# Kernel tuning notes

Measured on AMD Instinct MI355X. Metric: run time of the kernel, lower is better.

Reference implementation:

```python
import jax, jax.numpy as jnp
import numpy as np

B, S, DM, H, D = 2, 1024, 1024, 16, 64  # batch, seq, d_model, heads, head_dim


def setup_inputs() -> dict:
    key = jax.random.key(0)
    ks = jax.random.split(key, 16)
    sc = 1.0 / np.sqrt(DM)
    scd = 1.0 / np.sqrt(D)
    return {
        "hidden_states": jax.random.normal(ks[0], (B, S, DM), dtype=jnp.float32),
        # frozen base_attn projections
        "Wq": jax.random.normal(ks[1], (DM, DM), dtype=jnp.float32) * sc,
        "bq": jnp.zeros((DM,), dtype=jnp.float32),
        "Wk": jax.random.normal(ks[2], (DM, DM), dtype=jnp.float32) * sc,
        "bk": jnp.zeros((DM,), dtype=jnp.float32),
        "Wv": jax.random.normal(ks[3], (DM, DM), dtype=jnp.float32) * sc,
        "bv": jnp.zeros((DM,), dtype=jnp.float32),
        "Wo": jax.random.normal(ks[4], (DM, DM), dtype=jnp.float32) * sc,
        "bo": jnp.zeros((DM,), dtype=jnp.float32),
        # trainable hedgehog feature maps (per-head Linear(head_dim, head_dim))
        "Wfq": jax.random.normal(ks[5], (D, D), dtype=jnp.float32) * scd,
        "bfq": jnp.zeros((D,), dtype=jnp.float32),
        "Wfk": jax.random.normal(ks[6], (D, D), dtype=jnp.float32) * scd,
        "bfk": jnp.zeros((D,), dtype=jnp.float32),
    }


def _heads(x):
    # (B, S, DM) -> (B, H, S, D)
    return x.reshape(B, S, H, D).transpose(0, 2, 1, 3)


def _feature_map(x, W, b):
    # HedgehogFeatureMap: Linear then concat(exp(x), exp(-x)) along last dim
    y = jnp.einsum('bhsd,ed->bhse', x, W) + b
    return jnp.concatenate([jnp.exp(y), jnp.exp(-y)], axis=-1)  # (B,H,S,2D)


def reference(hidden_states, Wq, bq, Wk, bk, Wv, bv, Wo, bo, Wfq, bfq, Wfk, bfk):
    # base_attn: standard multi-head softmax attention with output_attentions=True
    q = _heads(hidden_states @ Wq.T + bq)
    k = _heads(hidden_states @ Wk.T + bk)
    v = _heads(hidden_states @ Wv.T + bv)
    scores = jnp.einsum('bhmd,bhnd->bhmn', q, k) / jnp.sqrt(jnp.float32(D))
    true_attns = jax.nn.softmax(scores, axis=-1)  # (B,H,S,S)
    ctx = jnp.einsum('bhmn,bhnd->bhmd', true_attns, v)
    outputs = ctx.transpose(0, 2, 1, 3).reshape(B, S, DM) @ Wo.T + bo

    # hedgehog path: feature maps on q/k then sum-normalized quadratic attention
    fq = _feature_map(q, Wfq, bfq)
    fk = _feature_map(k, Wfk, bfk)
    qk = jnp.einsum('bhmd,bhnd->bhmn', fq, fk)
    pred_attns = qk / jnp.sum(qk, axis=-1, keepdims=True)
    return (outputs, pred_attns, true_attns)
```

## Files before the change

kernel.cpp:

```cpp
#include <hip/hip_runtime.h>
#include <math.h>

constexpr int B_ = 2, S_ = 1024, DM_ = 1024, NH_ = 16, HD_ = 64;
constexpr long SD = (long)S_ * DM_;
constexpr long SS = (long)S_ * S_;

typedef _Float16 half8 __attribute__((ext_vector_type(8)));
typedef _Float16 half4 __attribute__((ext_vector_type(4)));
typedef float floatx4 __attribute__((ext_vector_type(4)));

__device__ __forceinline__ void gl_lds16(const void* g, void* l) {
    __builtin_amdgcn_global_load_lds(
        (const __attribute__((address_space(1))) void*)g,
        (__attribute__((address_space(3))) void*)l, 16, 0, 0);
}

__global__ __launch_bounds__(256) void cvt_all(
    const float* __restrict__ hs,  const float* __restrict__ Wq,
    const float* __restrict__ Wk,  const float* __restrict__ Wv,
    const float* __restrict__ Wo,  const float* __restrict__ Wfq,
    const float* __restrict__ Wfk,
    _Float16* __restrict__ hsH, _Float16* __restrict__ WqH,
    _Float16* __restrict__ WkH, _Float16* __restrict__ WvH,
    _Float16* __restrict__ WoH, _Float16* __restrict__ WfqH,
    _Float16* __restrict__ WfkH)
{
    long i = (long)blockIdx.x * 256 + threadIdx.x;
    const float* src; _Float16* dst; long off;
    if (i < 524288)       { src = hs;  dst = hsH;  off = i; }
    else if (i < 786432)  { src = Wq;  dst = WqH;  off = i - 524288; }
    else if (i < 1048576) { src = Wk;  dst = WkH;  off = i - 786432; }
    else if (i < 1310720) { src = Wv;  dst = WvH;  off = i - 1048576; }
    else if (i < 1572864) { src = Wo;  dst = WoH;  off = i - 1310720; }
    else if (i < 1573888) { src = Wfq; dst = WfqH; off = i - 1572864; }
    else                  { src = Wfk; dst = WfkH; off = i - 1573888; }
    float4 v = ((const float4*)src)[off];
    half4 h = { (_Float16)v.x, (_Float16)v.y, (_Float16)v.z, (_Float16)v.w };
    ((half4*)dst)[off] = h;
}

template <int BM, int BN, int WM, int WN>
__global__ __launch_bounds__(256) void mm_nt(
    const _Float16* __restrict__ Ap, const _Float16* __restrict__ Wp,
    const float* __restrict__ bias, const float* __restrict__ skp,
    float* __restrict__ Cf,
    _Float16* __restrict__ Ch, int K, int lda, int ldw, int ldc,
    long sAb, long sAh, long sWb, long sWh, long sCb, long sCh,
    float scale, int mode)
{
    constexpr int MI = WM / 16, NI = WN / 16;
    const int z = blockIdx.z, b = z / NH_, h = z % NH_;
    const int wave = threadIdx.x >> 6, lane = threadIdx.x & 63;
    const int m0 = blockIdx.y * BM, n0 = blockIdx.x * BN;
    const int wm = (wave >> 1) * WM, wn = (wave & 1) * WN;
    const int r16 = lane & 15, quad = lane >> 4;

    const _Float16* Az = Ap + (long)b * sAb + (long)h * sAh;
    const _Float16* Wz = Wp + (long)b * sWb + (long)h * sWh;

    __shared__ __align__(16) _Float16 As[2 * BM * 32];
    __shared__ __align__(16) _Float16 Bs[2 * BN * 32];
    __shared__ float skz[128];
    __shared__ float rsinvs[BM];

    if (skp) {
        if (threadIdx.x < 128) {
            float s = 0.f;
#pragma unroll
            for (int m = 0; m < 16; ++m)
                s += skp[((long)z * 16 + m) * 128 + threadIdx.x];
            skz[threadIdx.x] = s;
        }
        __syncthreads();
        if (threadIdx.x < BM) {
            const _Float16* p = Az + (long)(m0 + threadIdx.x) * lda;
            float acc = 0.f;
#pragma unroll
            for (int d0 = 0; d0 < 128; d0 += 8) {
                half8 v = *(const half8*)(p + d0);
#pragma unroll
                for (int j = 0; j < 8; ++j)
                    acc = fmaf((float)v[j], skz[d0 + j], acc);
            }
            rsinvs[threadIdx.x] = 1.f / acc;
        }
    }

    floatx4 acc[MI][NI];
#pragma unroll
    for (int i = 0; i < MI; ++i)
#pragma unroll
        for (int j = 0; j < NI; ++j)
#pragma unroll
            for (int r = 0; r < 4; ++r) acc[i][j][r] = 0.f;

    for (int k0 = 0; k0 < K; k0 += 64) {
#pragma unroll
        for (int hf = 0; hf < 2; ++hf) {
#pragma unroll
            for (int c = wave * (BM / 64); c < (wave + 1) * (BM / 64); ++c) {
                const _Float16* g = Az + (long)(m0 + c * 16 + (lane >> 2)) * lda
                                    + k0 + hf * 32 + (lane & 3) * 8;
                gl_lds16(g, &As[hf * BM * 32 + c * 512]);
            }
#pragma unroll
            for (int c = wave * (BN / 64); c < (wave + 1) * (BN / 64); ++c) {
                const _Float16* g = Wz + (long)(n0 + c * 16 + (lane >> 2)) * ldw
                                    + k0 + hf * 32 + (lane & 3) * 8;
                gl_lds16(g, &Bs[hf * BN * 32 + c * 512]);
            }
        }
        __syncthreads();

#pragma unroll
        for (int hf = 0; hf < 2; ++hf) {
            half8 af[MI], bf8[NI];
#pragma unroll
            for (int i = 0; i < MI; ++i)
                af[i] = *(const half8*)&As[hf * BM * 32
                                           + (wm + i * 16 + r16) * 32 + quad * 8];
#pragma unroll
            for (int j = 0; j < NI; ++j)
                bf8[j] = *(const half8*)&Bs[hf * BN * 32
                                            + (wn + j * 16 + r16) * 32 + quad * 8];
#pragma unroll
            for (int i = 0; i < MI; ++i)
#pragma unroll
                for (int j = 0; j < NI; ++j)
                    acc[i][j] = __builtin_amdgcn_mfma_f32_16x16x32_f16(
                        af[i], bf8[j], acc[i][j], 0, 0, 0);
        }
        __syncthreads();
    }

    const long cb = (long)b * sCb + (long)h * sCh;
#pragma unroll
    for (int i = 0; i < MI; ++i) {
#pragma unroll
        for (int j = 0; j < NI; ++j) {
#pragma unroll
            for (int r = 0; r < 4; ++r) {
                int row = m0 + wm + i * 16 + quad * 4 + r;
                int col = n0 + wn + j * 16 + r16;
                float v = acc[i][j][r] * scale;
                if (bias) v += bias[col];
                if (skp) v *= rsinvs[row - m0];
                if (mode == 0)
                    __builtin_nontemporal_store(v, &Cf[cb + (long)row * ldc + col]);
                else
                    Ch[cb + (long)row * ldc + col] = (_Float16)v;
            }
        }
    }
}

__global__ __launch_bounds__(256) void qkv_proj(
    const _Float16* __restrict__ hsH,
    const _Float16* __restrict__ W0, const _Float16* __restrict__ W1,
    const _Float16* __restrict__ W2,
    const float* __restrict__ b0, const float* __restrict__ b1,
    const float* __restrict__ b2,
    _Float16* __restrict__ QH, _Float16* __restrict__ KH,
    _Float16* __restrict__ VtH)
{
    const int z = blockIdx.z;
    const _Float16* W = (z == 0) ? W0 : (z == 1) ? W1 : W2;
    const float* bias = (z == 0) ? b0 : (z == 1) ? b1 : b2;

    const int wave = threadIdx.x >> 6, lane = threadIdx.x & 63;
    const int m0 = blockIdx.y * 64, n0 = blockIdx.x * 128;
    const int wm = (wave >> 1) * 32, wn = (wave & 1) * 64;
    const int r16 = lane & 15, quad = lane >> 4;

    __shared__ __align__(16) _Float16 As[2 * 64 * 32];
    __shared__ __align__(16) _Float16 Bs[2 * 128 * 32];

    floatx4 acc[2][4];
#pragma unroll
    for (int i = 0; i < 2; ++i)
#pragma unroll
        for (int j = 0; j < 4; ++j)
#pragma unroll
            for (int r = 0; r < 4; ++r) acc[i][j][r] = 0.f;

    for (int k0 = 0; k0 < 1024; k0 += 64) {
#pragma unroll
        for (int hf = 0; hf < 2; ++hf) {
            const _Float16* ga = hsH + (long)(m0 + wave * 16 + (lane >> 2)) * 1024
                                 + k0 + hf * 32 + (lane & 3) * 8;
            gl_lds16(ga, &As[hf * 2048 + wave * 512]);
#pragma unroll
            for (int c = wave * 2; c < wave * 2 + 2; ++c) {
                const _Float16* gb = W + (long)(n0 + c * 16 + (lane >> 2)) * 1024
                                     + k0 + hf * 32 + (lane & 3) * 8;
                gl_lds16(gb, &Bs[hf * 4096 + c * 512]);
            }
        }
        __syncthreads();

#pragma unroll
        for (int hf = 0; hf < 2; ++hf) {
            half8 af[2], bf8[4];
#pragma unroll
            for (int i = 0; i < 2; ++i)
                af[i] = *(const half8*)&As[hf * 2048
                                           + (wm + i * 16 + r16) * 32 + quad * 8];
#pragma unroll
            for (int j = 0; j < 4; ++j)
                bf8[j] = *(const half8*)&Bs[hf * 4096
                                            + (wn + j * 16 + r16) * 32 + quad * 8];
#pragma unroll
            for (int i = 0; i < 2; ++i)
#pragma unroll
                for (int j = 0; j < 4; ++j)
                    acc[i][j] = __builtin_amdgcn_mfma_f32_16x16x32_f16(
                        af[i], bf8[j], acc[i][j], 0, 0, 0);
        }
        __syncthreads();
    }

    _Float16* dst = (z == 0) ? QH : KH;
#pragma unroll
    for (int i = 0; i < 2; ++i) {
#pragma unroll
        for (int j = 0; j < 4; ++j) {
#pragma unroll
            for (int r = 0; r < 4; ++r) {
                int row = m0 + wm + i * 16 + quad * 4 + r;
                int col = n0 + wn + j * 16 + r16;
                float v = acc[i][j][r] + bias[col];
                if (z < 2) {
                    dst[(long)row * 1024 + col] = (_Float16)v;
                } else {
                    int bb = row >> 10, s = row & 1023;
                    int hh = col >> 6, d = col & 63;
                    VtH[((((long)bb * 16 + hh) * 64 + d) << 10) | s] = (_Float16)v;
                }
            }
        }
    }
}

__global__ __launch_bounds__(512) void attn_fused(
    const _Float16* __restrict__ Q, const _Float16* __restrict__ K,
    const _Float16* __restrict__ Vt, float* __restrict__ trueA,
    _Float16* __restrict__ ctx)
{
    const int z = blockIdx.y, b = z >> 4, h = z & 15;
    const int m0 = blockIdx.x * 32;
    const int wave = threadIdx.x >> 6, lane = threadIdx.x & 63;
    const int r16 = lane & 15, quad = lane >> 4;
    const int c0 = wave * 128;

    __shared__ __align__(16) _Float16 Ps[32 * 1024];
    float* redmx = (float*)Ps;
    float* redsm = (float*)Ps + 256;

    const _Float16* Qb = Q + (long)b * SD + h * 64;
    const _Float16* Kb = K + (long)b * SD + h * 64;

    half8 af[2][2];
#pragma unroll
    for (int mi = 0; mi < 2; ++mi)
#pragma unroll
        for (int ks = 0; ks < 2; ++ks)
            af[mi][ks] = *(const half8*)&Qb[(long)(m0 + mi * 16 + r16) * DM_
                                            + ks * 32 + quad * 8];

    floatx4 acc[2][8];
#pragma unroll
    for (int mi = 0; mi < 2; ++mi)
#pragma unroll
        for (int nj = 0; nj < 8; ++nj)
#pragma unroll
            for (int r = 0; r < 4; ++r) acc[mi][nj][r] = 0.f;

#pragma unroll
    for (int ks = 0; ks < 2; ++ks) {
#pragma unroll
        for (int nj = 0; nj < 8; ++nj) {
            half8 bf = *(const half8*)&Kb[(long)(c0 + nj * 16 + r16) * DM_
                                          + ks * 32 + quad * 8];
            acc[0][nj] = __builtin_amdgcn_mfma_f32_16x16x32_f16(
                af[0][ks], bf, acc[0][nj], 0, 0, 0);
            acc[1][nj] = __builtin_amdgcn_mfma_f32_16x16x32_f16(
                af[1][ks], bf, acc[1][nj], 0, 0, 0);
        }
    }

    float rmx[2][4];
#pragma unroll
    for (int mi = 0; mi < 2; ++mi)
#pragma unroll
        for (int r = 0; r < 4; ++r) {
            float m = acc[mi][0][r];
#pragma unroll
            for (int nj = 1; nj < 8; ++nj) m = fmaxf(m, acc[mi][nj][r]);
#pragma unroll
            for (int o = 1; o <= 8; o <<= 1) m = fmaxf(m, __shfl_xor(m, o, 64));
            rmx[mi][r] = m;
        }
    if (r16 == 0) {
#pragma unroll
        for (int mi = 0; mi < 2; ++mi)
#pragma unroll
            for (int r = 0; r < 4; ++r)
                redmx[wave * 32 + mi * 16 + quad * 4 + r] = rmx[mi][r];
    }
    __syncthreads();
    float mx[2][4];
#pragma unroll
    for (int mi = 0; mi < 2; ++mi)
#pragma unroll
        for (int r = 0; r < 4; ++r) {
            float m = redmx[mi * 16 + quad * 4 + r];
#pragma unroll
            for (int w = 1; w < 8; ++w)
                m = fmaxf(m, redmx[w * 32 + mi * 16 + quad * 4 + r]);
            mx[mi][r] = m;
        }

    float rsm[2][4];
#pragma unroll
    for (int mi = 0; mi < 2; ++mi)
#pragma unroll
        for (int r = 0; r < 4; ++r) {
            float s = 0.f;
#pragma unroll
            for (int nj = 0; nj < 8; ++nj) {
                float p = __expf((acc[mi][nj][r] - mx[mi][r]) * 0.125f);
                acc[mi][nj][r] = p;
                s += p;
            }
#pragma unroll
            for (int o = 1; o <= 8; o <<= 1) s += __shfl_xor(s, o, 64);
            rsm[mi][r] = s;
        }
    if (r16 == 0) {
#pragma unroll
        for (int mi = 0; mi < 2; ++mi)
#pragma unroll
            for (int r = 0; r < 4; ++r)
                redsm[wave * 32 + mi * 16 + quad * 4 + r] = rsm[mi][r];
    }
    __syncthreads();
    float inv[2][4];
#pragma unroll
    for (int mi = 0; mi < 2; ++mi)
#pragma unroll
        for (int r = 0; r < 4; ++r) {
            float s = 0.f;
#pragma unroll
            for (int w = 0; w < 8; ++w)
                s += redsm[w * 32 + mi * 16 + quad * 4 + r];
            inv[mi][r] = 1.f / s;
        }
    __syncthreads();

    float* Ta = trueA + (long)z * SS + (long)m0 * S_;
#pragma unroll
    for (int mi = 0; mi < 2; ++mi) {
#pragma unroll
        for (int r = 0; r < 4; ++r) {
            const int row = mi * 16 + quad * 4 + r;
            const int sw = (row & 7) << 3;
            const float iv = inv[mi][r];
#pragma unroll
            for (int nj = 0; nj < 8; ++nj) {
                const int col = c0 + nj * 16 + r16;
                const float v = acc[mi][nj][r] * iv;
                __builtin_nontemporal_store(v, &Ta[(long)row * S_ + col]);
                Ps[row * 1024 + (col ^ sw)] = (_Float16)v;
            }
        }
    }
    __syncthreads();

    const int mi = wave >> 2, d0 = (wave & 3) * 16;
    const _Float16* Vb = Vt + ((long)z * 64 + d0 + r16) * (long)S_;
    floatx4 c2;
#pragma unroll
    for (int r = 0; r < 4; ++r) c2[r] = 0.f;

    const int swz = (r16 & 7) << 3;
#pragma unroll 8
    for (int k0 = 0; k0 < 1024; k0 += 32) {
        half8 pa = *(const half8*)&Ps[(mi * 16 + r16) * 1024
                                      + ((k0 + quad * 8) ^ swz)];
        half8 vf = *(const half8*)&Vb[k0 + quad * 8];
        c2 = __builtin_amdgcn_mfma_f32_16x16x32_f16(pa, vf, c2, 0, 0, 0);
    }

    _Float16* Cb = ctx + (long)b * SD + h * 64;
#pragma unroll
    for (int r = 0; r < 4; ++r) {
        const int srow = m0 + mi * 16 + quad * 4 + r;
        Cb[(long)srow * DM_ + d0 + r16] = (_Float16)c2[r];
    }
}

__global__ __launch_bounds__(256) void feat_map2(
    const _Float16* __restrict__ QH, const _Float16* __restrict__ KH,
    const _Float16* __restrict__ Wfq, const _Float16* __restrict__ Wfk,
    const float* __restrict__ bfq, const float* __restrict__ bfk,
    _Float16* __restrict__ fqH, _Float16* __restrict__ fkH,
    float* __restrict__ skp)
{
    const int which = blockIdx.z;
    const _Float16* Xh = which ? KH : QH;
    const _Float16* Wf = which ? Wfk : Wfq;
    const float* bf    = which ? bfk : bfq;
    _Float16* outH     = which ? fkH : fqH;

    const int z = blockIdx.y, b = z >> 4, h = z & 15;
    const int mb = blockIdx.x, m0 = mb * 64;
    __shared__ float Xs[64][65];
    __shared__ float Ws[64][65];
    __shared__ float red[16][128];
    const _Float16* Xb = Xh + (long)b * SD + h * 64;
    for (int i = threadIdx.x; i < 4096; i += 256) {
        int r = i >> 6, c = i & 63;
        Xs[r][c] = (float)Xb[(long)(m0 + r) * 1024 + c];
        Ws[r][c] = (float)Wf[i];
    }
    __syncthreads();
    const int tmg = threadIdx.x >> 4;
    const int tm = tmg * 4, tn = (threadIdx.x & 15) * 4;
    float acc[4][4] = {{0.f}};
    for (int k = 0; k < 64; ++k) {
        float xv[4], wv[4];
#pragma unroll
        for (int i = 0; i < 4; ++i) xv[i] = Xs[tm + i][k];
#pragma unroll
        for (int j = 0; j < 4; ++j) wv[j] = Ws[tn + j][k];
#pragma unroll
        for (int i = 0; i < 4; ++i)
#pragma unroll
            for (int j = 0; j < 4; ++j) acc[i][j] = fmaf(xv[i], wv[j], acc[i][j]);
    }
    float sp[4] = {0.f, 0.f, 0.f, 0.f}, sn[4] = {0.f, 0.f, 0.f, 0.f};
#pragma unroll
    for (int i = 0; i < 4; ++i) {
        long base = ((long)z * S_ + m0 + tm + i) * 128;
#pragma unroll
        for (int j = 0; j < 4; ++j) {
            float y = acc[i][j] + bf[tn + j];
            float ep = expf(y), en = expf(-y);
            outH[base + tn + j]      = (_Float16)ep;
            outH[base + 64 + tn + j] = (_Float16)en;
            sp[j] += ep; sn[j] += en;
        }
    }
    if (which) {
#pragma unroll
        for (int j = 0; j < 4; ++j) {
            red[tmg][tn + j]      = sp[j];
            red[tmg][64 + tn + j] = sn[j];
        }
        __syncthreads();
        if (threadIdx.x < 128) {
            float s = 0.f;
#pragma unroll
            for (int g = 0; g < 16; ++g) s += red[g][threadIdx.x];
            skp[((long)z * 16 + mb) * 128 + threadIdx.x] = s;
        }
    }
}

extern "C" void kernel_launch(void* const* d_in, const int* in_sizes, int n_in,
                              void* d_out, int out_size, void* d_ws, size_t ws_size,
                              hipStream_t stream)
{
    (void)in_sizes; (void)n_in; (void)out_size; (void)ws_size;

    const float* hs  = (const float*)d_in[0];
    const float* Wq  = (const float*)d_in[1];
    const float* bq  = (const float*)d_in[2];
    const float* Wk  = (const float*)d_in[3];
    const float* bk  = (const float*)d_in[4];
    const float* Wv  = (const float*)d_in[5];
    const float* bv  = (const float*)d_in[6];
    const float* Wo  = (const float*)d_in[7];
    const float* bo  = (const float*)d_in[8];
    const float* Wfq = (const float*)d_in[9];
    const float* bfq = (const float*)d_in[10];
    const float* Wfk = (const float*)d_in[11];
    const float* bfk = (const float*)d_in[12];

    float* out0  = (float*)d_out;
    float* pred  = out0 + (long)B_ * S_ * DM_;
    float* trueA = pred + (long)B_ * NH_ * S_ * S_;

    _Float16* hsH  = (_Float16*)d_ws;
    _Float16* WqH  = hsH + 2 * 1024 * 1024;
    _Float16* WkH  = WqH + 1024 * 1024;
    _Float16* WvH  = WkH + 1024 * 1024;
    _Float16* WoH  = WvH + 1024 * 1024;
    _Float16* WfqH = WoH + 1024 * 1024;
    _Float16* WfkH = WfqH + 4096;
    _Float16* QH   = WfkH + 4096;
    _Float16* KH   = QH + 2 * 1024 * 1024;
    _Float16* VtH  = KH + 2 * 1024 * 1024;
    _Float16* ctxH = VtH + 2 * 1024 * 1024;
    _Float16* fqH  = ctxH + 2 * 1024 * 1024;
    _Float16* fkH  = fqH + (long)B_ * NH_ * S_ * 128;

    float* skp = (float*)WqH;

    const dim3 blk(256);

    cvt_all<<<6152, blk, 0, stream>>>(
        hs, Wq, Wk, Wv, Wo, Wfq, Wfk,
        hsH, WqH, WkH, WvH, WoH, WfqH, WfkH);

    qkv_proj<<<dim3(8, 32, 3), blk, 0, stream>>>(
        hsH, WqH, WkH, WvH, bq, bk, bv, QH, KH, VtH);

    attn_fused<<<dim3(32, 32), dim3(512), 0, stream>>>(
        QH, KH, VtH, trueA, ctxH);

    mm_nt<64, 64, 32, 32><<<dim3(16, 32, 1), blk, 0, stream>>>(
        ctxH, WoH, bo, nullptr, out0, nullptr, 1024, 1024, 1024, 1024,
        0, 0, 0, 0, 0, 0, 1.f, 0);

    feat_map2<<<dim3(16, 32, 2), blk, 0, stream>>>(
        QH, KH, WfqH, WfkH, bfq, bfk, fqH, fkH, skp);

    mm_nt<128, 128, 64, 64><<<dim3(8, 8, 32), blk, 0, stream>>>(
        fqH, fkH, nullptr, skp, pred, nullptr, 128, 128, 128, 1024,
        (long)16 * S_ * 128, (long)S_ * 128,
        (long)16 * S_ * 128, (long)S_ * 128,
        16 * SS, SS, 1.f, 0);
}
```

Baseline: 457.3 us.

## Swap MFMA operand order to get row-contiguous outputs and vectorized stores

Swaps the A/B operands of the MFMA calls in the GEMM, QKV projection and attention kernels, so each lane holds four consecutive columns of one row instead of four rows of one column. The epilogues become 16-byte float4 nontemporal stores and 8-byte half4 stores in place of scalar stores, and the softmax row reductions are reorganized to match (per-lane reduction plus two cross-quad shuffles instead of four shuffles per row). This targets store-bandwidth and instruction overhead, which matter most for the large fp32 attention-probability outputs. The transposed V store in the QKV kernel stays scalar.

Measured after the change: 448.8 us. Within noise of the previous version (-1.8%).

```diff
diff --git a/kernel.cpp b/kernel.cpp
--- a/kernel.cpp
+++ b/kernel.cpp
@@ -13,6 +13,10 @@
     __builtin_amdgcn_global_load_lds(
         (const __attribute__((address_space(1))) void*)g,
         (__attribute__((address_space(3))) void*)l, 16, 0, 0);
+}
+
+__device__ __forceinline__ void nt_store4(const floatx4& v, float* p) {
+    __builtin_nontemporal_store(v, (floatx4*)p);
 }
 
 __global__ __launch_bounds__(256) void cvt_all(
@@ -128,7 +132,7 @@
 #pragma unroll
                 for (int j = 0; j < NI; ++j)
                     acc[i][j] = __builtin_amdgcn_mfma_f32_16x16x32_f16(
-                        af[i], bf8[j], acc[i][j], 0, 0, 0);
+                        bf8[j], af[i], acc[i][j], 0, 0, 0);
         }
         __syncthreads();
     }
@@ -136,19 +140,28 @@
     const long cb = (long)b * sCb + (long)h * sCh;
 #pragma unroll
     for (int i = 0; i < MI; ++i) {
+        const int row = m0 + wm + i * 16 + r16;
+        const float rs = skp ? rsinvs[row - m0] : 1.f;
 #pragma unroll
         for (int j = 0; j < NI; ++j) {
-#pragma unroll
-            for (int r = 0; r < 4; ++r) {
-                int row = m0 + wm + i * 16 + quad * 4 + r;
-                int col = n0 + wn + j * 16 + r16;
-                float v = acc[i][j][r] * scale;
-                if (bias) v += bias[col];
-                if (skp) v *= rsinvs[row - m0];
-                if (mode == 0)
-                    __builtin_nontemporal_store(v, &Cf[cb + (long)row * ldc + col]);
-                else
-                    Ch[cb + (long)row * ldc + col] = (_Float16)v;
+            const int col = n0 + wn + j * 16 + quad * 4;
+            floatx4 v;
+#pragma unroll
+            for (int r = 0; r < 4; ++r) v[r] = acc[i][j][r] * scale;
+            if (bias) {
+                float4 bv = *(const float4*)&bias[col];
+                v[0] += bv.x; v[1] += bv.y; v[2] += bv.z; v[3] += bv.w;
+            }
+            if (skp) {
+#pragma unroll
+                for (int r = 0; r < 4; ++r) v[r] *= rs;
+            }
+            if (mode == 0) {
+                nt_store4(v, &Cf[cb + (long)row * ldc + col]);
+            } else {
+                half4 hv = { (_Float16)v[0], (_Float16)v[1],
+                             (_Float16)v[2], (_Float16)v[3] };
+                *(half4*)&Ch[cb + (long)row * ldc + col] = hv;
             }
         }
     }
@@ -214,7 +227,7 @@
 #pragma unroll
                 for (int j = 0; j < 4; ++j)
                     acc[i][j] = __builtin_amdgcn_mfma_f32_16x16x32_f16(
-                        af[i], bf8[j], acc[i][j], 0, 0, 0);
+                        bf8[j], af[i], acc[i][j], 0, 0, 0);
         }
         __syncthreads();
     }
@@ -222,20 +235,25 @@
     _Float16* dst = (z == 0) ? QH : KH;
 #pragma unroll
     for (int i = 0; i < 2; ++i) {
+        const int row = m0 + wm + i * 16 + r16;
 #pragma unroll
         for (int j = 0; j < 4; ++j) {
-#pragma unroll
-            for (int r = 0; r < 4; ++r) {
-                int row = m0 + wm + i * 16 + quad * 4 + r;
-                int col = n0 + wn + j * 16 + r16;
-                float v = acc[i][j][r] + bias[col];
-                if (z < 2) {
-                    dst[(long)row * 1024 + col] = (_Float16)v;
-                } else {
-                    int bb = row >> 10, s = row & 1023;
-                    int hh = col >> 6, d = col & 63;
-                    VtH[((((long)bb * 16 + hh) * 64 + d) << 10) | s] = (_Float16)v;
-                }
+            const int col = n0 + wn + j * 16 + quad * 4;
+            float4 bv = *(const float4*)&bias[col];
+            float v0 = acc[i][j][0] + bv.x, v1 = acc[i][j][1] + bv.y;
+            float v2 = acc[i][j][2] + bv.z, v3 = acc[i][j][3] + bv.w;
+            if (z < 2) {
+                half4 hv = { (_Float16)v0, (_Float16)v1,
+                             (_Float16)v2, (_Float16)v3 };
+                *(half4*)&dst[(long)row * 1024 + col] = hv;
+            } else {
+                const int bb = row >> 10, s = row & 1023;
+                const int hh = col >> 6, d0 = col & 63;
+                float vv[4] = { v0, v1, v2, v3 };
+#pragma unroll
+                for (int r = 0; r < 4; ++r)
+                    VtH[((((long)bb * 16 + hh) * 64 + d0 + r) << 10) | s] =
+                        (_Float16)vv[r];
             }
         }
     }
@@ -259,12 +277,12 @@
     const _Float16* Qb = Q + (long)b * SD + h * 64;
     const _Float16* Kb = K + (long)b * SD + h * 64;
 
-    half8 af[2][2];
+    half8 qf[2][2];
 #pragma unroll
     for (int mi = 0; mi < 2; ++mi)
 #pragma unroll
         for (int ks = 0; ks < 2; ++ks)
-            af[mi][ks] = *(const half8*)&Qb[(long)(m0 + mi * 16 + r16) * DM_
+            qf[mi][ks] = *(const half8*)&Qb[(long)(m0 + mi * 16 + r16) * DM_
                                             + ks * 32 + quad * 8];
 
     floatx4 acc[2][8];
@@ -279,99 +297,91 @@
     for (int ks = 0; ks < 2; ++ks) {
 #pragma unroll
         for (int nj = 0; nj < 8; ++nj) {
-            half8 bf = *(const half8*)&Kb[(long)(c0 + nj * 16 + r16) * DM_
+            half8 kf = *(const half8*)&Kb[(long)(c0 + nj * 16 + r16) * DM_
                                           + ks * 32 + quad * 8];
             acc[0][nj] = __builtin_amdgcn_mfma_f32_16x16x32_f16(
-                af[0][ks], bf, acc[0][nj], 0, 0, 0);
+                kf, qf[0][ks], acc[0][nj], 0, 0, 0);
             acc[1][nj] = __builtin_amdgcn_mfma_f32_16x16x32_f16(
-                af[1][ks], bf, acc[1][nj], 0, 0, 0);
-        }
-    }
-
-    float rmx[2][4];
-#pragma unroll
-    for (int mi = 0; mi < 2; ++mi)
-#pragma unroll
-        for (int r = 0; r < 4; ++r) {
-            float m = acc[mi][0][r];
-#pragma unroll
-            for (int nj = 1; nj < 8; ++nj) m = fmaxf(m, acc[mi][nj][r]);
-#pragma unroll
-            for (int o = 1; o <= 8; o <<= 1) m = fmaxf(m, __shfl_xor(m, o, 64));
-            rmx[mi][r] = m;
-        }
-    if (r16 == 0) {
-#pragma unroll
-        for (int mi = 0; mi < 2; ++mi)
-#pragma unroll
-            for (int r = 0; r < 4; ++r)
-                redmx[wave * 32 + mi * 16 + quad * 4 + r] = rmx[mi][r];
+                kf, qf[1][ks], acc[1][nj], 0, 0, 0);
+        }
+    }
+
+    float mxl[2];
+#pragma unroll
+    for (int mi = 0; mi < 2; ++mi) {
+        float m = acc[mi][0][0];
+#pragma unroll
+        for (int nj = 0; nj < 8; ++nj)
+#pragma unroll
+            for (int r = 0; r < 4; ++r) m = fmaxf(m, acc[mi][nj][r]);
+        m = fmaxf(m, __shfl_xor(m, 16, 64));
+        m = fmaxf(m, __shfl_xor(m, 32, 64));
+        mxl[mi] = m;
+    }
+    if (quad == 0) {
+        redmx[wave * 32 + r16]      = mxl[0];
+        redmx[wave * 32 + 16 + r16] = mxl[1];
     }
     __syncthreads();
-    float mx[2][4];
-#pragma unroll
-    for (int mi = 0; mi < 2; ++mi)
-#pragma unroll
-        for (int r = 0; r < 4; ++r) {
-            float m = redmx[mi * 16 + quad * 4 + r];
-#pragma unroll
-            for (int w = 1; w < 8; ++w)
-                m = fmaxf(m, redmx[w * 32 + mi * 16 + quad * 4 + r]);
-            mx[mi][r] = m;
-        }
-
-    float rsm[2][4];
-#pragma unroll
-    for (int mi = 0; mi < 2; ++mi)
-#pragma unroll
-        for (int r = 0; r < 4; ++r) {
-            float s = 0.f;
-#pragma unroll
-            for (int nj = 0; nj < 8; ++nj) {
-                float p = __expf((acc[mi][nj][r] - mx[mi][r]) * 0.125f);
+    float mx[2];
+#pragma unroll
+    for (int mi = 0; mi < 2; ++mi) {
+        float m = redmx[mi * 16 + r16];
+#pragma unroll
+        for (int w = 1; w < 8; ++w)
+            m = fmaxf(m, redmx[w * 32 + mi * 16 + r16]);
+        mx[mi] = m;
+    }
+
+    float sml[2];
+#pragma unroll
+    for (int mi = 0; mi < 2; ++mi) {
+        float s = 0.f;
+#pragma unroll
+        for (int nj = 0; nj < 8; ++nj)
+#pragma unroll
+            for (int r = 0; r < 4; ++r) {
+                float p = __expf((acc[mi][nj][r] - mx[mi]) * 0.125f);
                 acc[mi][nj][r] = p;
                 s += p;
             }
-#pragma unroll
-            for (int o = 1; o <= 8; o <<= 1) s += __shfl_xor(s, o, 64);
-            rsm[mi][r] = s;
-        }
-    if (r16 == 0) {
-#pragma unroll
-        for (int mi = 0; mi < 2; ++mi)
-#pragma unroll
-            for (int r = 0; r < 4; ++r)
-                redsm[wave * 32 + mi * 16 + quad * 4 + r] = rsm[mi][r];
+        s += __shfl_xor(s, 16, 64);
+        s += __shfl_xor(s, 32, 64);
+        sml[mi] = s;
+    }
+    if (quad == 0) {
+        redsm[wave * 32 + r16]      = sml[0];
+        redsm[wave * 32 + 16 + r16] = sml[1];
     }
     __syncthreads();
-    float inv[2][4];
-#pragma unroll
-    for (int mi = 0; mi < 2; ++mi)
-#pragma unroll
-        for (int r = 0; r < 4; ++r) {
-            float s = 0.f;
-#pragma unroll
-            for (int w = 0; w < 8; ++w)
-                s += redsm[w * 32 + mi * 16 + quad * 4 + r];
-            inv[mi][r] = 1.f / s;
-        }
+    float inv[2];
+#pragma unroll
+    for (int mi = 0; mi < 2; ++mi) {
+        float s = 0.f;
+#pragma unroll
+        for (int w = 0; w < 8; ++w) s += redsm[w * 32 + mi * 16 + r16];
+        inv[mi] = 1.f / s;
+    }
     __syncthreads();
 
     float* Ta = trueA + (long)z * SS + (long)m0 * S_;
+    const int sw = (r16 & 7) << 3;
 #pragma unroll
     for (int mi = 0; mi < 2; ++mi) {
-#pragma unroll
-        for (int r = 0; r < 4; ++r) {
-            const int row = mi * 16 + quad * 4 + r;
-            const int sw = (row & 7) << 3;
-            const float iv = inv[mi][r];
-#pragma unroll
-            for (int nj = 0; nj < 8; ++nj) {
-                const int col = c0 + nj * 16 + r16;
-                const float v = acc[mi][nj][r] * iv;
-                __builtin_nontemporal_store(v, &Ta[(long)row * S_ + col]);
-                Ps[row * 1024 + (col ^ sw)] = (_Float16)v;
-            }
+        const int row = mi * 16 + r16;
+        const float iv = inv[mi];
+#pragma unroll
+        for (int nj = 0; nj < 8; ++nj) {
+            const int col = c0 + nj * 16 + quad * 4;
+            floatx4 tv; half4 hv;
+#pragma unroll
+            for (int r = 0; r < 4; ++r) {
+                float v = acc[mi][nj][r] * iv;
+                tv[r] = v;
+                hv[r] = (_Float16)v;
+            }
+            nt_store4(tv, &Ta[(long)row * S_ + col]);
+            *(half4*)&Ps[row * 1024 + (col ^ sw)] = hv;
         }
     }
     __syncthreads();
@@ -388,15 +398,13 @@
         half8 pa = *(const half8*)&Ps[(mi * 16 + r16) * 1024
                                       + ((k0 + quad * 8) ^ swz)];
         half8 vf = *(const half8*)&Vb[k0 + quad * 8];
-        c2 = __builtin_amdgcn_mfma_f32_16x16x32_f16(pa, vf, c2, 0, 0, 0);
+        c2 = __builtin_amdgcn_mfma_f32_16x16x32_f16(vf, pa, c2, 0, 0, 0);
     }
 
     _Float16* Cb = ctx + (long)b * SD + h * 64;
-#pragma unroll
-    for (int r = 0; r < 4; ++r) {
-        const int srow = m0 + mi * 16 + quad * 4 + r;
-        Cb[(long)srow * DM_ + d0 + r16] = (_Float16)c2[r];
-    }
+    half4 cv = { (_Float16)c2[0], (_Float16)c2[1],
+                 (_Float16)c2[2], (_Float16)c2[3] };
+    *(half4*)&Cb[(long)(m0 + mi * 16 + r16) * DM_ + d0 + quad * 4] = cv;
 }
 
 __global__ __launch_bounds__(256) void feat_map2(
```
